# Optimization experiments

Measured on AMD Instinct MI355X. Metric: run time of the kernel, lower is better.

The kernel has to match this reference:

```python
import jax, jax.numpy as jnp
import numpy as np

B, CF, CC, H, W = 4, 64, 128, 512, 512
NUM_POINTS = 4096
OVERSAMPLE = 3
BETA = 0.75
HIDDEN = 256
OUT_CH = 4
IN_FEATS = CF + CC


def grid_sample_points(img, coords):
    """Bilinear sample img [B,C,H,W] at coords [B,N,2] in [0,1] (x,y order),
    matching F.grid_sample(align_corners=False, padding_mode='zeros') after
    the 2*coords-1 normalization in point_sample."""
    Bb, C, Hh, Ww = img.shape
    # unnormalize: ((2c-1)+1)*size/2 - 0.5 == c*size - 0.5
    x = coords[..., 0] * Ww - 0.5
    y = coords[..., 1] * Hh - 0.5
    x0 = jnp.floor(x)
    y0 = jnp.floor(y)
    wx1 = x - x0  # [B,N]
    wy1 = y - y0
    x0i = x0.astype(jnp.int32)
    y0i = y0.astype(jnp.int32)
    flat = img.reshape(Bb, C, Hh * Ww)

    def gather(xi, yi):
        valid = (xi >= 0) & (xi < Ww) & (yi >= 0) & (yi < Hh)
        idx = jnp.clip(yi, 0, Hh - 1) * Ww + jnp.clip(xi, 0, Ww - 1)
        v = jnp.take_along_axis(flat, idx[:, None, :], axis=2)  # [B,C,N]
        return v * valid[:, None, :].astype(img.dtype)

    out = (gather(x0i, y0i) * ((1.0 - wx1) * (1.0 - wy1))[:, None, :]
           + gather(x0i + 1, y0i) * (wx1 * (1.0 - wy1))[:, None, :]
           + gather(x0i, y0i + 1) * ((1.0 - wx1) * wy1)[:, None, :]
           + gather(x0i + 1, y0i + 1) * (wx1 * wy1)[:, None, :])
    return out  # [B,C,N]


def setup_inputs() -> dict:
    key = jax.random.key(0)
    ks = jax.random.split(key, 12)
    num_sampled = NUM_POINTS * OVERSAMPLE
    num_uncertain = int(BETA * NUM_POINTS)
    num_random = NUM_POINTS - num_uncertain
    s1 = 1.0 / np.sqrt(IN_FEATS)
    s2 = 1.0 / np.sqrt(HIDDEN)
    return {
        "fine_features": jax.random.normal(ks[0], (B, CF, H, W), jnp.float32),
        "coarse_features": jax.random.normal(ks[1], (B, CC, H, W), jnp.float32),
        "coarse_logits": jax.random.normal(ks[2], (B, OUT_CH, H, W), jnp.float32),
        "rand_points": jax.random.uniform(ks[3], (B, num_sampled, 2), jnp.float32),
        "rand_extra": jax.random.uniform(ks[4], (B, num_random, 2), jnp.float32),
        "W1": jax.random.uniform(ks[5], (HIDDEN, IN_FEATS), jnp.float32, -s1, s1),
        "b1": jax.random.uniform(ks[6], (HIDDEN,), jnp.float32, -s1, s1),
        "W2": jax.random.uniform(ks[7], (HIDDEN, HIDDEN), jnp.float32, -s2, s2),
        "b2": jax.random.uniform(ks[8], (HIDDEN,), jnp.float32, -s2, s2),
        "W3": jax.random.uniform(ks[9], (OUT_CH, HIDDEN), jnp.float32, -s2, s2),
        "b3": jax.random.uniform(ks[10], (OUT_CH,), jnp.float32, -s2, s2),
    }


def reference(fine_features, coarse_features, coarse_logits, rand_points,
              rand_extra, W1, b1, W2, b2, W3, b3):
    # 1) uncertainty at oversampled random points (channel 0 of coarse logits)
    pt_logits0 = grid_sample_points(coarse_logits, rand_points)[:, 0, :]  # [B,Ns]
    uncertainty = 1.0 - jnp.abs(jax.nn.sigmoid(pt_logits0) - 0.5) * 2.0
    num_uncertain = int(BETA * NUM_POINTS)
    _, idx = jax.lax.top_k(uncertainty, num_uncertain)  # [B,k]
    chosen_uncertain = jnp.take_along_axis(rand_points, idx[..., None], axis=1)
    points = jnp.concatenate([chosen_uncertain, rand_extra], axis=1)  # [B,N,2]
    # 2) gather fine + coarse features at selected points
    fine_s = grid_sample_points(fine_features, points)      # [B,Cf,N]
    coarse_s = grid_sample_points(coarse_features, points)  # [B,Cc,N]
    feats = jnp.concatenate([fine_s, coarse_s], axis=1).transpose(0, 2, 1)  # [B,N,Cin]
    # 3) pointwise MLP (torch Linear: x @ W.T + b)
    h = jax.nn.relu(feats @ W1.T + b1)
    h = jax.nn.relu(h @ W2.T + b2)
    point_logits = (h @ W3.T + b3).transpose(0, 2, 1)  # [B,out_ch,N]
    return point_logits, points
```

## Files before the change

kernel.cpp:

```cpp
#include <hip/hip_runtime.h>
#include <math.h>

#define BATCH 4
#define HW 512
#define NPLANE (512 * 512)
#define NS 12288
#define NU 3072
#define NR 1024
#define NP 4096
#define CF_CH 64
#define CC_CH 128
#define CIN 192
#define HID 256
#define OUTC 4
#define M_TOT (BATCH * NP)
#define GCH_SPLIT 4

__device__ __forceinline__ float xla_expf(float xin) {
  float x = fminf(fmaxf(xin, -88.3762626647949f), 88.3762626647950f);
  float fx = floorf(__fadd_rn(__fmul_rn(x, 1.44269504088896341f), 0.5f));
  float tmp = __fmul_rn(0.693359375f, fx);
  float z = __fmul_rn(-2.12194440e-4f, fx);
  x = __fsub_rn(__fsub_rn(x, tmp), z);
  float y = __fadd_rn(__fmul_rn(x, 1.9875691500E-4f), 1.3981999507E-3f);
  y = __fadd_rn(__fmul_rn(y, x), 8.3334519073E-3f);
  y = __fadd_rn(__fmul_rn(y, x), 4.1665795894E-2f);
  y = __fadd_rn(__fmul_rn(y, x), 1.6666665459E-1f);
  y = __fadd_rn(__fmul_rn(y, x), 5.0000001201E-1f);
  z = __fmul_rn(x, x);
  y = __fadd_rn(__fmul_rn(y, z), x);
  y = __fadd_rn(y, 1.0f);
  int n = (int)fx;
  float p2n = __int_as_float((n + 127) << 23);
  return __fmul_rn(y, p2n);
}

__global__ void k_uncert(const float* __restrict__ logits,
                         const float* __restrict__ rp,
                         float* __restrict__ u) {
  int gid = blockIdx.x * 256 + threadIdx.x;
  if (gid >= BATCH * NS) return;
  int b = gid / NS;
  float px = rp[(size_t)gid * 2 + 0];
  float py = rp[(size_t)gid * 2 + 1];
  const float* plane = logits + (size_t)b * OUTC * NPLANE;

  float x = __fsub_rn(__fmul_rn(px, 512.0f), 0.5f);
  float y = __fsub_rn(__fmul_rn(py, 512.0f), 0.5f);
  float x0f = floorf(x), y0f = floorf(y);
  float wx = __fsub_rn(x, x0f);
  float wy = __fsub_rn(y, y0f);
  int x0 = (int)x0f, y0 = (int)y0f;
  int x1 = x0 + 1, y1 = y0 + 1;
  bool vx0 = (x0 >= 0) & (x0 < HW);
  bool vx1 = (x1 >= 0) & (x1 < HW);
  bool vy0 = (y0 >= 0) & (y0 < HW);
  bool vy1 = (y1 >= 0) & (y1 < HW);
  float g00 = (vx0 && vy0) ? plane[y0 * HW + x0] : 0.0f;
  float g10 = (vx1 && vy0) ? plane[y0 * HW + x1] : 0.0f;
  float g01 = (vx0 && vy1) ? plane[y1 * HW + x0] : 0.0f;
  float g11 = (vx1 && vy1) ? plane[y1 * HW + x1] : 0.0f;
  float omx = __fsub_rn(1.0f, wx);
  float omy = __fsub_rn(1.0f, wy);
  float w00 = __fmul_rn(omx, omy);
  float w10 = __fmul_rn(wx, omy);
  float w01 = __fmul_rn(omx, wy);
  float w11 = __fmul_rn(wx, wy);
  float s = __fadd_rn(
      __fadd_rn(__fadd_rn(__fmul_rn(g00, w00), __fmul_rn(g10, w10)),
                __fmul_rn(g01, w01)),
      __fmul_rn(g11, w11));
  float e = xla_expf(-s);
  float sig = __fdiv_rn(1.0f, __fadd_rn(1.0f, e));
  float t = __fmul_rn(fabsf(__fsub_rn(sig, 0.5f)), 2.0f);
  u[gid] = __fsub_rn(1.0f, t);
}

__global__ __launch_bounds__(256) void k_select(const float* __restrict__ u,
                                                const float* __restrict__ rp,
                                                float* __restrict__ pts_out) {
  __shared__ __align__(16) float su[NS];
  int b = blockIdx.x / (NS / 256);
  int blk = blockIdx.x % (NS / 256);
  const float* ub = u + (size_t)b * NS;
  for (int t = threadIdx.x; t < NS / 4; t += 256)
    ((float4*)su)[t] = ((const float4*)ub)[t];
  __syncthreads();
  int i = blk * 256 + (int)threadIdx.x;
  int wb = i & ~63;
  float ui = su[i];
  int r0 = 0, r1 = 0, r2 = 0, r3 = 0;
  for (int j = 0; j < wb; j += 8) {
    float4 v = *(const float4*)&su[j];
    float4 w = *(const float4*)&su[j + 4];
    r0 += (v.x >= ui) + (w.x >= ui);
    r1 += (v.y >= ui) + (w.y >= ui);
    r2 += (v.z >= ui) + (w.z >= ui);
    r3 += (v.w >= ui) + (w.w >= ui);
  }
  for (int j = wb; j < wb + 64; ++j) {
    float vj = su[j];
    r0 += (vj > ui) || (vj == ui && j < i);
  }
  for (int j = wb + 64; j < NS; j += 8) {
    float4 v = *(const float4*)&su[j];
    float4 w = *(const float4*)&su[j + 4];
    r0 += (v.x > ui) + (w.x > ui);
    r1 += (v.y > ui) + (w.y > ui);
    r2 += (v.z > ui) + (w.z > ui);
    r3 += (v.w > ui) + (w.w > ui);
  }
  int rank = (r0 + r1) + (r2 + r3);
  if (rank < NU) {
    pts_out[((size_t)b * NP + rank) * 2 + 0] = rp[((size_t)b * NS + i) * 2 + 0];
    pts_out[((size_t)b * NP + rank) * 2 + 1] = rp[((size_t)b * NS + i) * 2 + 1];
  }
}

__global__ void k_extra(const float* __restrict__ re, float* __restrict__ pts_out) {
  int gid = blockIdx.x * 256 + threadIdx.x;
  if (gid >= BATCH * NR) return;
  int b = gid / NR, j = gid % NR;
  pts_out[((size_t)b * NP + NU + j) * 2 + 0] = re[(size_t)gid * 2 + 0];
  pts_out[((size_t)b * NP + NU + j) * 2 + 1] = re[(size_t)gid * 2 + 1];
}

__global__ void k_prep(const float* __restrict__ pts, int2* __restrict__ m2,
                       float4* __restrict__ wts) {
  int g = blockIdx.x * 256 + threadIdx.x;
  if (g >= M_TOT) return;
  float px = pts[(size_t)g * 2 + 0];
  float py = pts[(size_t)g * 2 + 1];
  float x = px * 512.0f - 0.5f;
  float y = py * 512.0f - 0.5f;
  float x0f = floorf(x), y0f = floorf(y);
  float wx = x - x0f, wy = y - y0f;
  int x0 = (int)x0f, y0 = (int)y0f;
  bool vx0 = (unsigned)x0 < (unsigned)HW;
  bool vx1 = (unsigned)(x0 + 1) < (unsigned)HW;
  bool vy0 = (unsigned)y0 < (unsigned)HW;
  bool vy1 = (unsigned)(y0 + 1) < (unsigned)HW;
  int vm = (int)(vx0 && vy0) | ((int)(vx1 && vy0) << 1) |
           ((int)(vx0 && vy1) << 2) | ((int)(vx1 && vy1) << 3);
  m2[g] = make_int2(y0 * HW + x0, vm);
  wts[g] = make_float4((1.0f - wx) * (1.0f - wy), wx * (1.0f - wy),
                       (1.0f - wx) * wy, wx * wy);
}

__global__ __launch_bounds__(512) void k_sort(const int2* __restrict__ m2,
                                              int* __restrict__ perm) {
  __shared__ int hist[512], pref[512];
  int b = blockIdx.x, tid = threadIdx.x;
  hist[tid] = 0;
  __syncthreads();
  for (int p = tid; p < NP; p += 512) {
    int i00 = m2[(size_t)b * NP + p].x;
    int key = min(max(i00, 0), NPLANE - 1) >> 9;
    atomicAdd(&hist[key], 1);
  }
  __syncthreads();
  int v = hist[tid];
  pref[tid] = v;
  __syncthreads();
  for (int d = 1; d < 512; d <<= 1) {
    int t = (tid >= d) ? pref[tid - d] : 0;
    __syncthreads();
    pref[tid] += t;
    __syncthreads();
  }
  hist[tid] = pref[tid] - v;
  __syncthreads();
  for (int p = tid; p < NP; p += 512) {
    int i00 = m2[(size_t)b * NP + p].x;
    int key = min(max(i00, 0), NPLANE - 1) >> 9;
    int pos = atomicAdd(&hist[key], 1);
    perm[(size_t)b * NP + pos] = p;
  }
}

__global__ void k_reorder(const int* __restrict__ perm,
                          const int2* __restrict__ m2,
                          const float4* __restrict__ wts,
                          int2* __restrict__ m2s, float4* __restrict__ wtss) {
  int gid = blockIdx.x * 256 + threadIdx.x;
  if (gid >= M_TOT) return;
  int b = gid / NP;
  int p = perm[gid];
  m2s[gid] = m2[(size_t)b * NP + p];
  wtss[gid] = wts[(size_t)b * NP + p];
}

__global__ __launch_bounds__(256) void k_gather5(
    const float* __restrict__ fine, const float* __restrict__ coarse,
    const int2* __restrict__ m2s, const float4* __restrict__ wtss,
    float* __restrict__ featsT) {
  int c = blockIdx.x % CIN;
  int rem = blockIdx.x / CIN;
  int b = rem & (BATCH - 1);
  int part = rem >> 2;
  const float* plane = (c < CF_CH)
                           ? fine + ((size_t)b * CF_CH + c) * NPLANE
                           : coarse + ((size_t)b * CC_CH + (c - CF_CH)) * NPLANE;
  const int2* m2b = m2s + (size_t)b * NP;
  const float4* wtsb = wtss + (size_t)b * NP;
  float* outrow = featsT + (size_t)c * M_TOT + (size_t)b * NP;
  int s0 = part * (NP / GCH_SPLIT);
#pragma unroll
  for (int q = 0; q < NP / GCH_SPLIT / 256; ++q) {
    int s = s0 + q * 256 + (int)threadIdx.x;
    int2 mm = m2b[s];
    float4 w = wtsb[s];
    const float* bp = plane + mm.x;
    float t00 = 0.0f, t10 = 0.0f, t01 = 0.0f, t11 = 0.0f;
    if (mm.y & 1) t00 = bp[0] * w.x;
    if (mm.y & 2) t10 = bp[1] * w.y;
    if (mm.y & 4) t01 = bp[HW] * w.z;
    if (mm.y & 8) t11 = bp[HW + 1] * w.w;
    outrow[s] = ((t00 + t10) + t01) + t11;
  }
}

__global__ __launch_bounds__(256) void k_gemm1_At(const float* __restrict__ At,
                                                  const float* __restrict__ W,
                                                  const float* __restrict__ bias,
                                                  float* __restrict__ C) {
  __shared__ __align__(16) float As[32][68];
  __shared__ __align__(16) float Bs[32][68];
  const int bx = blockIdx.x & 3;
  const int by = blockIdx.x >> 2;
  const int tid = threadIdx.x;
  const int tn = tid & 15, tm = tid >> 4;
  const int m_base = by * 64, n_base = bx * 64;
  float acc[4][4] = {};
  for (int k0 = 0; k0 < CIN; k0 += 32) {
#pragma unroll
    for (int r = 0; r < 2; ++r) {
      int t = tid + r * 256;
      int kk = t >> 4, mg = (t & 15) * 4;
      *(float4*)&As[kk][mg] =
          *(const float4*)&At[(size_t)(k0 + kk) * M_TOT + m_base + mg];
      int row = t >> 3, cg = (t & 7) * 4;
      float4 vw = *(const float4*)&W[(size_t)(n_base + row) * CIN + k0 + cg];
      Bs[cg + 0][row] = vw.x;
      Bs[cg + 1][row] = vw.y;
      Bs[cg + 2][row] = vw.z;
      Bs[cg + 3][row] = vw.w;
    }
    __syncthreads();
#pragma unroll
    for (int kk = 0; kk < 32; ++kk) {
      float4 a4 = *(const float4*)&As[kk][tm * 4];
      float4 b4 = *(const float4*)&Bs[kk][tn * 4];
      float av[4] = {a4.x, a4.y, a4.z, a4.w};
      float bw[4] = {b4.x, b4.y, b4.z, b4.w};
#pragma unroll
      for (int i = 0; i < 4; ++i)
#pragma unroll
        for (int j = 0; j < 4; ++j) acc[i][j] = fmaf(av[i], bw[j], acc[i][j]);
    }
    __syncthreads();
  }
  float bs[4];
#pragma unroll
  for (int j = 0; j < 4; ++j) bs[j] = bias[n_base + tn * 4 + j];
#pragma unroll
  for (int i = 0; i < 4; ++i) {
    float4 o;
    o.x = fmaxf(acc[i][0] + bs[0], 0.0f);
    o.y = fmaxf(acc[i][1] + bs[1], 0.0f);
    o.z = fmaxf(acc[i][2] + bs[2], 0.0f);
    o.w = fmaxf(acc[i][3] + bs[3], 0.0f);
    *(float4*)&C[(size_t)(m_base + tm * 4 + i) * HID + n_base + tn * 4] = o;
  }
}

template <int K>
__global__ __launch_bounds__(256) void k_gemm_relu(const float* __restrict__ A,
                                                   const float* __restrict__ W,
                                                   const float* __restrict__ bias,
                                                   float* __restrict__ C) {
  __shared__ __align__(16) float As[32][68];
  __shared__ __align__(16) float Bs[32][68];
  const int bx = blockIdx.x & 3;
  const int by = blockIdx.x >> 2;
  const int tid = threadIdx.x;
  const int tn = tid & 15, tm = tid >> 4;
  const int m_base = by * 64, n_base = bx * 64;
  float acc[4][4] = {};
  for (int k0 = 0; k0 < K; k0 += 32) {
#pragma unroll
    for (int r = 0; r < 2; ++r) {
      int t = tid + r * 256;
      int row = t >> 3, cg = (t & 7) * 4;
      float4 va = *(const float4*)&A[(size_t)(m_base + row) * K + k0 + cg];
      As[cg + 0][row] = va.x;
      As[cg + 1][row] = va.y;
      As[cg + 2][row] = va.z;
      As[cg + 3][row] = va.w;
      float4 vw = *(const float4*)&W[(size_t)(n_base + row) * K + k0 + cg];
      Bs[cg + 0][row] = vw.x;
      Bs[cg + 1][row] = vw.y;
      Bs[cg + 2][row] = vw.z;
      Bs[cg + 3][row] = vw.w;
    }
    __syncthreads();
#pragma unroll
    for (int kk = 0; kk < 32; ++kk) {
      float4 a4 = *(const float4*)&As[kk][tm * 4];
      float4 b4 = *(const float4*)&Bs[kk][tn * 4];
      float av[4] = {a4.x, a4.y, a4.z, a4.w};
      float bw[4] = {b4.x, b4.y, b4.z, b4.w};
#pragma unroll
      for (int i = 0; i < 4; ++i)
#pragma unroll
        for (int j = 0; j < 4; ++j) acc[i][j] = fmaf(av[i], bw[j], acc[i][j]);
    }
    __syncthreads();
  }
  float bs[4];
#pragma unroll
  for (int j = 0; j < 4; ++j) bs[j] = bias[n_base + tn * 4 + j];
#pragma unroll
  for (int i = 0; i < 4; ++i) {
    float4 o;
    o.x = fmaxf(acc[i][0] + bs[0], 0.0f);
    o.y = fmaxf(acc[i][1] + bs[1], 0.0f);
    o.z = fmaxf(acc[i][2] + bs[2], 0.0f);
    o.w = fmaxf(acc[i][3] + bs[3], 0.0f);
    *(float4*)&C[(size_t)(m_base + tm * 4 + i) * HID + n_base + tn * 4] = o;
  }
}

__global__ __launch_bounds__(256) void k_out(const float* __restrict__ h,
                                             const float* __restrict__ W3,
                                             const float* __restrict__ b3,
                                             const int* __restrict__ perm,
                                             float* __restrict__ out) {
  int gp = blockIdx.x * 4 + (threadIdx.x >> 6);
  int lane = threadIdx.x & 63;
  const float* hr = h + (size_t)gp * HID;
  float4 hv = *(const float4*)&hr[lane * 4];
  float s[4];
#pragma unroll
  for (int o = 0; o < 4; ++o) {
    float4 w = *(const float4*)&W3[o * HID + lane * 4];
    s[o] = hv.x * w.x + hv.y * w.y + hv.z * w.z + hv.w * w.w;
  }
#pragma unroll
  for (int off = 32; off; off >>= 1)
#pragma unroll
    for (int o = 0; o < 4; ++o) s[o] += __shfl_xor(s[o], off, 64);
  if (lane == 0) {
    int b = gp / NP, ns = gp % NP;
    int n = perm[(size_t)b * NP + ns];
#pragma unroll
    for (int o = 0; o < 4; ++o)
      out[((size_t)b * OUTC + o) * NP + n] = s[o] + b3[o];
  }
}

extern "C" void kernel_launch(void* const* d_in, const int* in_sizes, int n_in,
                              void* d_out, int out_size, void* d_ws, size_t ws_size,
                              hipStream_t stream) {
  const float* fine = (const float*)d_in[0];
  const float* coarse = (const float*)d_in[1];
  const float* logits = (const float*)d_in[2];
  const float* rand_points = (const float*)d_in[3];
  const float* rand_extra = (const float*)d_in[4];
  const float* W1 = (const float*)d_in[5];
  const float* b1 = (const float*)d_in[6];
  const float* W2 = (const float*)d_in[7];
  const float* b2 = (const float*)d_in[8];
  const float* W3 = (const float*)d_in[9];
  const float* b3 = (const float*)d_in[10];
  float* out = (float*)d_out;

  float* out_logits = out;
  float* out_points = out + (size_t)BATCH * OUTC * NP;

  char* ws = (char*)d_ws;
  float* u = (float*)(ws + 0);
  int2* m2 = (int2*)(ws + 196608);
  float4* wts = (float4*)(ws + 327680);
  int2* m2s = (int2*)(ws + 589824);
  float4* wtss = (float4*)(ws + 720896);
  int* perm = (int*)(ws + 983040);
  float* featsT = (float*)(ws + 1048576);
  float* h1 = (float*)(ws + 13631488);
  float* h2 = (float*)(ws + 30408704);

  k_uncert<<<(BATCH * NS + 255) / 256, 256, 0, stream>>>(logits, rand_points, u);
  k_select<<<BATCH * (NS / 256), 256, 0, stream>>>(u, rand_points, out_points);
  k_extra<<<(BATCH * NR + 255) / 256, 256, 0, stream>>>(rand_extra, out_points);
  k_prep<<<(M_TOT + 255) / 256, 256, 0, stream>>>(out_points, m2, wts);
  k_sort<<<BATCH, 512, 0, stream>>>(m2, perm);
  k_reorder<<<(M_TOT + 255) / 256, 256, 0, stream>>>(perm, m2, wts, m2s, wtss);
  k_gather5<<<CIN * BATCH * GCH_SPLIT, 256, 0, stream>>>(fine, coarse, m2s,
                                                         wtss, featsT);
  k_gemm1_At<<<(M_TOT / 64) * 4, 256, 0, stream>>>(featsT, W1, b1, h1);
  k_gemm_relu<HID><<<(M_TOT / 64) * 4, 256, 0, stream>>>(h1, W2, b2, h2);
  k_out<<<M_TOT / 4, 256, 0, stream>>>(h2, W3, b3, perm, out_logits);
}
```

Baseline: 306.0 us.

## Run MLP GEMMs on bf16 MFMA with hi/lo split-precision operands

Replaces the two FP32 SIMT shared-memory GEMMs with MFMA bf16 kernels. Each operand is split into high and low bf16 parts and three MFMAs per tile approximate FP32 accuracy. New conversion kernels transpose and split the gathered features and weights, and the first GEMM writes its output already split for the second. This adds extra launches, extra conversion traffic, and direct global loads with no LDS staging, in exchange for matrix-core throughput.

```diff
diff --git a/kernel.cpp b/kernel.cpp
--- a/kernel.cpp
+++ b/kernel.cpp
@@ -15,6 +15,18 @@
 #define OUTC 4
 #define M_TOT (BATCH * NP)
 #define GCH_SPLIT 4
+
+typedef __attribute__((ext_vector_type(8))) short bf16x8;
+typedef __attribute__((ext_vector_type(4))) float f32x4;
+
+__device__ __forceinline__ unsigned short f32_to_bf16_rne(float f) {
+  unsigned u = __float_as_uint(f);
+  unsigned r = u + 0x7FFFu + ((u >> 16) & 1u);
+  return (unsigned short)(r >> 16);
+}
+__device__ __forceinline__ float bf16_to_f32(unsigned short h) {
+  return __uint_as_float((unsigned)h << 16);
+}
 
 __device__ __forceinline__ float xla_expf(float xin) {
   float x = fminf(fmaxf(xin, -88.3762626647949f), 88.3762626647950f);
@@ -220,114 +232,99 @@
   }
 }
 
-__global__ __launch_bounds__(256) void k_gemm1_At(const float* __restrict__ At,
-                                                  const float* __restrict__ W,
-                                                  const float* __restrict__ bias,
-                                                  float* __restrict__ C) {
-  __shared__ __align__(16) float As[32][68];
-  __shared__ __align__(16) float Bs[32][68];
-  const int bx = blockIdx.x & 3;
-  const int by = blockIdx.x >> 2;
-  const int tid = threadIdx.x;
-  const int tn = tid & 15, tm = tid >> 4;
-  const int m_base = by * 64, n_base = bx * 64;
-  float acc[4][4] = {};
-  for (int k0 = 0; k0 < CIN; k0 += 32) {
-#pragma unroll
-    for (int r = 0; r < 2; ++r) {
-      int t = tid + r * 256;
-      int kk = t >> 4, mg = (t & 15) * 4;
-      *(float4*)&As[kk][mg] =
-          *(const float4*)&At[(size_t)(k0 + kk) * M_TOT + m_base + mg];
-      int row = t >> 3, cg = (t & 7) * 4;
-      float4 vw = *(const float4*)&W[(size_t)(n_base + row) * CIN + k0 + cg];
-      Bs[cg + 0][row] = vw.x;
-      Bs[cg + 1][row] = vw.y;
-      Bs[cg + 2][row] = vw.z;
-      Bs[cg + 3][row] = vw.w;
+__global__ __launch_bounds__(256) void k_convA(const float* __restrict__ featsT,
+                                               unsigned short* __restrict__ AH,
+                                               unsigned short* __restrict__ AL) {
+  __shared__ float t[32][65];
+  int c0 = (blockIdx.x % (CIN / 32)) * 32;
+  int m0 = (blockIdx.x / (CIN / 32)) * 64;
+#pragma unroll
+  for (int it = 0; it < 8; ++it) {
+    int idx = it * 256 + (int)threadIdx.x;
+    int cl = idx >> 6, ml = idx & 63;
+    t[cl][ml] = featsT[(size_t)(c0 + cl) * M_TOT + m0 + ml];
+  }
+  __syncthreads();
+#pragma unroll
+  for (int it = 0; it < 8; ++it) {
+    int idx = it * 256 + (int)threadIdx.x;
+    int ml = idx >> 5, cl = idx & 31;
+    float f = t[cl][ml];
+    unsigned short h = f32_to_bf16_rne(f);
+    unsigned short l = f32_to_bf16_rne(f - bf16_to_f32(h));
+    AH[(size_t)(m0 + ml) * CIN + c0 + cl] = h;
+    AL[(size_t)(m0 + ml) * CIN + c0 + cl] = l;
+  }
+}
+
+__global__ void k_convW(const float* __restrict__ W,
+                        unsigned short* __restrict__ WH,
+                        unsigned short* __restrict__ WL, int n) {
+  int g = blockIdx.x * 256 + threadIdx.x;
+  if (g >= n) return;
+  float f = W[g];
+  unsigned short h = f32_to_bf16_rne(f);
+  WH[g] = h;
+  WL[g] = f32_to_bf16_rne(f - bf16_to_f32(h));
+}
+
+template <int K, bool SPLIT>
+__global__ __launch_bounds__(256) void k_mfma(
+    const unsigned short* __restrict__ AH, const unsigned short* __restrict__ AL,
+    const unsigned short* __restrict__ BH, const unsigned short* __restrict__ BL,
+    const float* __restrict__ bias, float* __restrict__ outF,
+    unsigned short* __restrict__ outH, unsigned short* __restrict__ outL) {
+  int lane = (int)threadIdx.x & 63, w = (int)threadIdx.x >> 6;
+  int m0 = blockIdx.y * 64 + (w >> 1) * 32;
+  int n0 = blockIdx.x * 64 + (w & 1) * 32;
+  int rA = lane & 15, kg = (lane >> 4) * 8;
+  f32x4 acc00 = {}, acc01 = {}, acc10 = {}, acc11 = {};
+  for (int kc = 0; kc < K; kc += 32) {
+    int k = kc + kg;
+    bf16x8 ah0 = *(const bf16x8*)&AH[(size_t)(m0 + rA) * K + k];
+    bf16x8 ah1 = *(const bf16x8*)&AH[(size_t)(m0 + 16 + rA) * K + k];
+    bf16x8 al0 = *(const bf16x8*)&AL[(size_t)(m0 + rA) * K + k];
+    bf16x8 al1 = *(const bf16x8*)&AL[(size_t)(m0 + 16 + rA) * K + k];
+    bf16x8 bh0 = *(const bf16x8*)&BH[(size_t)(n0 + rA) * K + k];
+    bf16x8 bh1 = *(const bf16x8*)&BH[(size_t)(n0 + 16 + rA) * K + k];
+    bf16x8 bl0 = *(const bf16x8*)&BL[(size_t)(n0 + rA) * K + k];
+    bf16x8 bl1 = *(const bf16x8*)&BL[(size_t)(n0 + 16 + rA) * K + k];
+    acc00 = __builtin_amdgcn_mfma_f32_16x16x32_bf16(ah0, bh0, acc00, 0, 0, 0);
+    acc00 = __builtin_amdgcn_mfma_f32_16x16x32_bf16(ah0, bl0, acc00, 0, 0, 0);
+    acc00 = __builtin_amdgcn_mfma_f32_16x16x32_bf16(al0, bh0, acc00, 0, 0, 0);
+    acc01 = __builtin_amdgcn_mfma_f32_16x16x32_bf16(ah0, bh1, acc01, 0, 0, 0);
+    acc01 = __builtin_amdgcn_mfma_f32_16x16x32_bf16(ah0, bl1, acc01, 0, 0, 0);
+    acc01 = __builtin_amdgcn_mfma_f32_16x16x32_bf16(al0, bh1, acc01, 0, 0, 0);
+    acc10 = __builtin_amdgcn_mfma_f32_16x16x32_bf16(ah1, bh0, acc10, 0, 0, 0);
+    acc10 = __builtin_amdgcn_mfma_f32_16x16x32_bf16(ah1, bl0, acc10, 0, 0, 0);
+    acc10 = __builtin_amdgcn_mfma_f32_16x16x32_bf16(al1, bh0, acc10, 0, 0, 0);
+    acc11 = __builtin_amdgcn_mfma_f32_16x16x32_bf16(ah1, bh1, acc11, 0, 0, 0);
+    acc11 = __builtin_amdgcn_mfma_f32_16x16x32_bf16(ah1, bl1, acc11, 0, 0, 0);
+    acc11 = __builtin_amdgcn_mfma_f32_16x16x32_bf16(al1, bh1, acc11, 0, 0, 0);
+  }
+  int cr = (lane >> 4) * 4;
+  int cc = lane & 15;
+  float b0 = bias[n0 + cc], b1v = bias[n0 + 16 + cc];
+#pragma unroll
+  for (int r = 0; r < 4; ++r) {
+#pragma unroll
+    for (int fi = 0; fi < 2; ++fi) {
+      int row = m0 + fi * 16 + cr + r;
+      float v0 = fmaxf((fi ? acc10[r] : acc00[r]) + b0, 0.0f);
+      float v1 = fmaxf((fi ? acc11[r] : acc01[r]) + b1v, 0.0f);
+      if constexpr (SPLIT) {
+        unsigned short h0 = f32_to_bf16_rne(v0);
+        unsigned short h1 = f32_to_bf16_rne(v1);
+        outH[(size_t)row * HID + n0 + cc] = h0;
+        outH[(size_t)row * HID + n0 + 16 + cc] = h1;
+        outL[(size_t)row * HID + n0 + cc] = f32_to_bf16_rne(v0 - bf16_to_f32(h0));
+        outL[(size_t)row * HID + n0 + 16 + cc] =
+            f32_to_bf16_rne(v1 - bf16_to_f32(h1));
+      } else {
+        outF[(size_t)row * HID + n0 + cc] = v0;
+        outF[(size_t)row * HID + n0 + 16 + cc] = v1;
+      }
     }
-    __syncthreads();
-#pragma unroll
-    for (int kk = 0; kk < 32; ++kk) {
-      float4 a4 = *(const float4*)&As[kk][tm * 4];
-      float4 b4 = *(const float4*)&Bs[kk][tn * 4];
-      float av[4] = {a4.x, a4.y, a4.z, a4.w};
-      float bw[4] = {b4.x, b4.y, b4.z, b4.w};
-#pragma unroll
-      for (int i = 0; i < 4; ++i)
-#pragma unroll
-        for (int j = 0; j < 4; ++j) acc[i][j] = fmaf(av[i], bw[j], acc[i][j]);
-    }
-    __syncthreads();
-  }
-  float bs[4];
-#pragma unroll
-  for (int j = 0; j < 4; ++j) bs[j] = bias[n_base + tn * 4 + j];
-#pragma unroll
-  for (int i = 0; i < 4; ++i) {
-    float4 o;
-    o.x = fmaxf(acc[i][0] + bs[0], 0.0f);
-    o.y = fmaxf(acc[i][1] + bs[1], 0.0f);
-    o.z = fmaxf(acc[i][2] + bs[2], 0.0f);
-    o.w = fmaxf(acc[i][3] + bs[3], 0.0f);
-    *(float4*)&C[(size_t)(m_base + tm * 4 + i) * HID + n_base + tn * 4] = o;
-  }
-}
-
-template <int K>
-__global__ __launch_bounds__(256) void k_gemm_relu(const float* __restrict__ A,
-                                                   const float* __restrict__ W,
-                                                   const float* __restrict__ bias,
-                                                   float* __restrict__ C) {
-  __shared__ __align__(16) float As[32][68];
-  __shared__ __align__(16) float Bs[32][68];
-  const int bx = blockIdx.x & 3;
-  const int by = blockIdx.x >> 2;
-  const int tid = threadIdx.x;
-  const int tn = tid & 15, tm = tid >> 4;
-  const int m_base = by * 64, n_base = bx * 64;
-  float acc[4][4] = {};
-  for (int k0 = 0; k0 < K; k0 += 32) {
-#pragma unroll
-    for (int r = 0; r < 2; ++r) {
-      int t = tid + r * 256;
-      int row = t >> 3, cg = (t & 7) * 4;
-      float4 va = *(const float4*)&A[(size_t)(m_base + row) * K + k0 + cg];
-      As[cg + 0][row] = va.x;
-      As[cg + 1][row] = va.y;
-      As[cg + 2][row] = va.z;
-      As[cg + 3][row] = va.w;
-      float4 vw = *(const float4*)&W[(size_t)(n_base + row) * K + k0 + cg];
-      Bs[cg + 0][row] = vw.x;
-      Bs[cg + 1][row] = vw.y;
-      Bs[cg + 2][row] = vw.z;
-      Bs[cg + 3][row] = vw.w;
-    }
-    __syncthreads();
-#pragma unroll
-    for (int kk = 0; kk < 32; ++kk) {
-      float4 a4 = *(const float4*)&As[kk][tm * 4];
-      float4 b4 = *(const float4*)&Bs[kk][tn * 4];
-      float av[4] = {a4.x, a4.y, a4.z, a4.w};
-      float bw[4] = {b4.x, b4.y, b4.z, b4.w};
-#pragma unroll
-      for (int i = 0; i < 4; ++i)
-#pragma unroll
-        for (int j = 0; j < 4; ++j) acc[i][j] = fmaf(av[i], bw[j], acc[i][j]);
-    }
-    __syncthreads();
-  }
-  float bs[4];
-#pragma unroll
-  for (int j = 0; j < 4; ++j) bs[j] = bias[n_base + tn * 4 + j];
-#pragma unroll
-  for (int i = 0; i < 4; ++i) {
-    float4 o;
-    o.x = fmaxf(acc[i][0] + bs[0], 0.0f);
-    o.y = fmaxf(acc[i][1] + bs[1], 0.0f);
-    o.z = fmaxf(acc[i][2] + bs[2], 0.0f);
-    o.w = fmaxf(acc[i][3] + bs[3], 0.0f);
-    *(float4*)&C[(size_t)(m_base + tm * 4 + i) * HID + n_base + tn * 4] = o;
   }
 }
 
@@ -386,10 +383,19 @@
   float4* wtss = (float4*)(ws + 720896);
   int* perm = (int*)(ws + 983040);
   float* featsT = (float*)(ws + 1048576);
-  float* h1 = (float*)(ws + 13631488);
-  float* h2 = (float*)(ws + 30408704);
+  unsigned short* AH = (unsigned short*)(ws + 13631488);
+  unsigned short* AL = (unsigned short*)(ws + 19922944);
+  unsigned short* W1H = (unsigned short*)(ws + 26214400);
+  unsigned short* W1L = (unsigned short*)(ws + 26312704);
+  unsigned short* W2H = (unsigned short*)(ws + 26411008);
+  unsigned short* W2L = (unsigned short*)(ws + 26542080);
+  unsigned short* h1H = (unsigned short*)(ws + 26673152);
+  unsigned short* h1L = (unsigned short*)(ws + 35061760);
+  float* h2 = (float*)(ws + 43450368);
 
   k_uncert<<<(BATCH * NS + 255) / 256, 256, 0, stream>>>(logits, rand_points, u);
+  k_convW<<<(HID * CIN + 255) / 256, 256, 0, stream>>>(W1, W1H, W1L, HID * CIN);
+  k_convW<<<(HID * HID + 255) / 256, 256, 0, stream>>>(W2, W2H, W2L, HID * HID);
   k_select<<<BATCH * (NS / 256), 256, 0, stream>>>(u, rand_points, out_points);
   k_extra<<<(BATCH * NR + 255) / 256, 256, 0, stream>>>(rand_extra, out_points);
   k_prep<<<(M_TOT + 255) / 256, 256, 0, stream>>>(out_points, m2, wts);
@@ -397,7 +403,10 @@
   k_reorder<<<(M_TOT + 255) / 256, 256, 0, stream>>>(perm, m2, wts, m2s, wtss);
   k_gather5<<<CIN * BATCH * GCH_SPLIT, 256, 0, stream>>>(fine, coarse, m2s,
                                                          wtss, featsT);
-  k_gemm1_At<<<(M_TOT / 64) * 4, 256, 0, stream>>>(featsT, W1, b1, h1);
-  k_gemm_relu<HID><<<(M_TOT / 64) * 4, 256, 0, stream>>>(h1, W2, b2, h2);
+  k_convA<<<(CIN / 32) * (M_TOT / 64), 256, 0, stream>>>(featsT, AH, AL);
+  k_mfma<CIN, true><<<dim3(HID / 64, M_TOT / 64), 256, 0, stream>>>(
+      AH, AL, W1H, W1L, b1, nullptr, h1H, h1L);
+  k_mfma<HID, false><<<dim3(HID / 64, M_TOT / 64), 256, 0, stream>>>(
+      h1H, h1L, W2H, W2L, b2, h2, nullptr, nullptr);
   k_out<<<M_TOT / 4, 256, 0, stream>>>(h2, W3, b3, perm, out_logits);
 }
```

New measurement: 315.5 us. +3.1%, slower.

## Fuse second MLP GEMM with output projection and merge extra-points copy into uncertainty kernel

Applied to the files above, without the earlier changes.

The second hidden-layer GEMM now computes a full 64x256 tile per block and applies bias, ReLU and the 4-channel output projection in registers. Partial sums are reduced with shuffles, so the h2 buffer round trip and the separate k_out launch go away. The rand_extra copy is folded into the uncertainty kernel, removing one more launch. In exchange the GEMM grid shrinks from 1024 to 256 blocks, each with 64 accumulators per thread and a larger shared tile, which may reduce occupancy and parallelism.

```diff
diff --git a/kernel.cpp b/kernel.cpp
--- a/kernel.cpp
+++ b/kernel.cpp
@@ -35,45 +35,55 @@
   return __fmul_rn(y, p2n);
 }
 
-__global__ void k_uncert(const float* __restrict__ logits,
-                         const float* __restrict__ rp,
-                         float* __restrict__ u) {
+__global__ void k_uncert_extra(const float* __restrict__ logits,
+                               const float* __restrict__ rp,
+                               const float* __restrict__ re,
+                               float* __restrict__ u,
+                               float* __restrict__ pts_out) {
   int gid = blockIdx.x * 256 + threadIdx.x;
-  if (gid >= BATCH * NS) return;
-  int b = gid / NS;
-  float px = rp[(size_t)gid * 2 + 0];
-  float py = rp[(size_t)gid * 2 + 1];
-  const float* plane = logits + (size_t)b * OUTC * NPLANE;
-
-  float x = __fsub_rn(__fmul_rn(px, 512.0f), 0.5f);
-  float y = __fsub_rn(__fmul_rn(py, 512.0f), 0.5f);
-  float x0f = floorf(x), y0f = floorf(y);
-  float wx = __fsub_rn(x, x0f);
-  float wy = __fsub_rn(y, y0f);
-  int x0 = (int)x0f, y0 = (int)y0f;
-  int x1 = x0 + 1, y1 = y0 + 1;
-  bool vx0 = (x0 >= 0) & (x0 < HW);
-  bool vx1 = (x1 >= 0) & (x1 < HW);
-  bool vy0 = (y0 >= 0) & (y0 < HW);
-  bool vy1 = (y1 >= 0) & (y1 < HW);
-  float g00 = (vx0 && vy0) ? plane[y0 * HW + x0] : 0.0f;
-  float g10 = (vx1 && vy0) ? plane[y0 * HW + x1] : 0.0f;
-  float g01 = (vx0 && vy1) ? plane[y1 * HW + x0] : 0.0f;
-  float g11 = (vx1 && vy1) ? plane[y1 * HW + x1] : 0.0f;
-  float omx = __fsub_rn(1.0f, wx);
-  float omy = __fsub_rn(1.0f, wy);
-  float w00 = __fmul_rn(omx, omy);
-  float w10 = __fmul_rn(wx, omy);
-  float w01 = __fmul_rn(omx, wy);
-  float w11 = __fmul_rn(wx, wy);
-  float s = __fadd_rn(
-      __fadd_rn(__fadd_rn(__fmul_rn(g00, w00), __fmul_rn(g10, w10)),
-                __fmul_rn(g01, w01)),
-      __fmul_rn(g11, w11));
-  float e = xla_expf(-s);
-  float sig = __fdiv_rn(1.0f, __fadd_rn(1.0f, e));
-  float t = __fmul_rn(fabsf(__fsub_rn(sig, 0.5f)), 2.0f);
-  u[gid] = __fsub_rn(1.0f, t);
+  if (gid < BATCH * NS) {
+    int b = gid / NS;
+    float px = rp[(size_t)gid * 2 + 0];
+    float py = rp[(size_t)gid * 2 + 1];
+    const float* plane = logits + (size_t)b * OUTC * NPLANE;
+
+    float x = __fsub_rn(__fmul_rn(px, 512.0f), 0.5f);
+    float y = __fsub_rn(__fmul_rn(py, 512.0f), 0.5f);
+    float x0f = floorf(x), y0f = floorf(y);
+    float wx = __fsub_rn(x, x0f);
+    float wy = __fsub_rn(y, y0f);
+    int x0 = (int)x0f, y0 = (int)y0f;
+    int x1 = x0 + 1, y1 = y0 + 1;
+    bool vx0 = (x0 >= 0) & (x0 < HW);
+    bool vx1 = (x1 >= 0) & (x1 < HW);
+    bool vy0 = (y0 >= 0) & (y0 < HW);
+    bool vy1 = (y1 >= 0) & (y1 < HW);
+    float g00 = (vx0 && vy0) ? plane[y0 * HW + x0] : 0.0f;
+    float g10 = (vx1 && vy0) ? plane[y0 * HW + x1] : 0.0f;
+    float g01 = (vx0 && vy1) ? plane[y1 * HW + x0] : 0.0f;
+    float g11 = (vx1 && vy1) ? plane[y1 * HW + x1] : 0.0f;
+    float omx = __fsub_rn(1.0f, wx);
+    float omy = __fsub_rn(1.0f, wy);
+    float w00 = __fmul_rn(omx, omy);
+    float w10 = __fmul_rn(wx, omy);
+    float w01 = __fmul_rn(omx, wy);
+    float w11 = __fmul_rn(wx, wy);
+    float s = __fadd_rn(
+        __fadd_rn(__fadd_rn(__fmul_rn(g00, w00), __fmul_rn(g10, w10)),
+                  __fmul_rn(g01, w01)),
+        __fmul_rn(g11, w11));
+    float e = xla_expf(-s);
+    float sig = __fdiv_rn(1.0f, __fadd_rn(1.0f, e));
+    float t = __fmul_rn(fabsf(__fsub_rn(sig, 0.5f)), 2.0f);
+    u[gid] = __fsub_rn(1.0f, t);
+  } else {
+    int g = gid - BATCH * NS;
+    if (g < BATCH * NR) {
+      int b = g / NR, j = g - b * NR;
+      pts_out[((size_t)b * NP + NU + j) * 2 + 0] = re[(size_t)g * 2 + 0];
+      pts_out[((size_t)b * NP + NU + j) * 2 + 1] = re[(size_t)g * 2 + 1];
+    }
+  }
 }
 
 __global__ __launch_bounds__(256) void k_select(const float* __restrict__ u,
@@ -117,14 +127,6 @@
   }
 }
 
-__global__ void k_extra(const float* __restrict__ re, float* __restrict__ pts_out) {
-  int gid = blockIdx.x * 256 + threadIdx.x;
-  if (gid >= BATCH * NR) return;
-  int b = gid / NR, j = gid % NR;
-  pts_out[((size_t)b * NP + NU + j) * 2 + 0] = re[(size_t)gid * 2 + 0];
-  pts_out[((size_t)b * NP + NU + j) * 2 + 1] = re[(size_t)gid * 2 + 1];
-}
-
 __global__ void k_prep(const float* __restrict__ pts, int2* __restrict__ m2,
                        float4* __restrict__ wts) {
   int g = blockIdx.x * 256 + threadIdx.x;
@@ -274,30 +276,36 @@
   }
 }
 
-template <int K>
-__global__ __launch_bounds__(256) void k_gemm_relu(const float* __restrict__ A,
-                                                   const float* __restrict__ W,
-                                                   const float* __restrict__ bias,
-                                                   float* __restrict__ C) {
+__global__ __launch_bounds__(256) void k_gemm2_fused(
+    const float* __restrict__ A,
+    const float* __restrict__ W,
+    const float* __restrict__ bias,
+    const float* __restrict__ W3,
+    const float* __restrict__ b3,
+    const int* __restrict__ perm,
+    float* __restrict__ out) {
   __shared__ __align__(16) float As[32][68];
-  __shared__ __align__(16) float Bs[32][68];
-  const int bx = blockIdx.x & 3;
-  const int by = blockIdx.x >> 2;
+  __shared__ __align__(16) float Bs[32][260];
   const int tid = threadIdx.x;
-  const int tn = tid & 15, tm = tid >> 4;
-  const int m_base = by * 64, n_base = bx * 64;
-  float acc[4][4] = {};
-  for (int k0 = 0; k0 < K; k0 += 32) {
+  const int tm = tid >> 4, tn = tid & 15;
+  const int m_base = blockIdx.x * 64;
+  float acc[4][16] = {};
+  for (int k0 = 0; k0 < HID; k0 += 32) {
 #pragma unroll
     for (int r = 0; r < 2; ++r) {
       int t = tid + r * 256;
       int row = t >> 3, cg = (t & 7) * 4;
-      float4 va = *(const float4*)&A[(size_t)(m_base + row) * K + k0 + cg];
+      float4 va = *(const float4*)&A[(size_t)(m_base + row) * HID + k0 + cg];
       As[cg + 0][row] = va.x;
       As[cg + 1][row] = va.y;
       As[cg + 2][row] = va.z;
       As[cg + 3][row] = va.w;
-      float4 vw = *(const float4*)&W[(size_t)(n_base + row) * K + k0 + cg];
+    }
+#pragma unroll
+    for (int r = 0; r < 8; ++r) {
+      int t = tid + r * 256;
+      int row = t >> 3, cg = (t & 7) * 4;
+      float4 vw = *(const float4*)&W[(size_t)row * HID + k0 + cg];
       Bs[cg + 0][row] = vw.x;
       Bs[cg + 1][row] = vw.y;
       Bs[cg + 2][row] = vw.z;
@@ -306,56 +314,51 @@
     __syncthreads();
 #pragma unroll
     for (int kk = 0; kk < 32; ++kk) {
-      float4 a4 = *(const float4*)&As[kk][tm * 4];
-      float4 b4 = *(const float4*)&Bs[kk][tn * 4];
-      float av[4] = {a4.x, a4.y, a4.z, a4.w};
-      float bw[4] = {b4.x, b4.y, b4.z, b4.w};
+      float a4[4];
+      *(float4*)a4 = *(const float4*)&As[kk][tm * 4];
+      float bw[16];
+#pragma unroll
+      for (int j = 0; j < 4; ++j)
+        *(float4*)&bw[j * 4] = *(const float4*)&Bs[kk][tn * 16 + j * 4];
 #pragma unroll
       for (int i = 0; i < 4; ++i)
 #pragma unroll
-        for (int j = 0; j < 4; ++j) acc[i][j] = fmaf(av[i], bw[j], acc[i][j]);
-    }
-    __syncthreads();
-  }
-  float bs[4];
-#pragma unroll
-  for (int j = 0; j < 4; ++j) bs[j] = bias[n_base + tn * 4 + j];
-#pragma unroll
-  for (int i = 0; i < 4; ++i) {
-    float4 o;
-    o.x = fmaxf(acc[i][0] + bs[0], 0.0f);
-    o.y = fmaxf(acc[i][1] + bs[1], 0.0f);
-    o.z = fmaxf(acc[i][2] + bs[2], 0.0f);
-    o.w = fmaxf(acc[i][3] + bs[3], 0.0f);
-    *(float4*)&C[(size_t)(m_base + tm * 4 + i) * HID + n_base + tn * 4] = o;
-  }
-}
-
-__global__ __launch_bounds__(256) void k_out(const float* __restrict__ h,
-                                             const float* __restrict__ W3,
-                                             const float* __restrict__ b3,
-                                             const int* __restrict__ perm,
-                                             float* __restrict__ out) {
-  int gp = blockIdx.x * 4 + (threadIdx.x >> 6);
-  int lane = threadIdx.x & 63;
-  const float* hr = h + (size_t)gp * HID;
-  float4 hv = *(const float4*)&hr[lane * 4];
-  float s[4];
-#pragma unroll
-  for (int o = 0; o < 4; ++o) {
-    float4 w = *(const float4*)&W3[o * HID + lane * 4];
-    s[o] = hv.x * w.x + hv.y * w.y + hv.z * w.z + hv.w * w.w;
-  }
-#pragma unroll
-  for (int off = 32; off; off >>= 1)
-#pragma unroll
-    for (int o = 0; o < 4; ++o) s[o] += __shfl_xor(s[o], off, 64);
-  if (lane == 0) {
-    int b = gp / NP, ns = gp % NP;
-    int n = perm[(size_t)b * NP + ns];
-#pragma unroll
-    for (int o = 0; o < 4; ++o)
-      out[((size_t)b * OUTC + o) * NP + n] = s[o] + b3[o];
+        for (int j = 0; j < 16; ++j)
+          acc[i][j] = fmaf(a4[i], bw[j], acc[i][j]);
+    }
+    __syncthreads();
+  }
+  float p[4][4] = {};
+#pragma unroll
+  for (int j = 0; j < 16; ++j) {
+    int n = tn * 16 + j;
+    float bn = bias[n];
+    float w3v[4];
+#pragma unroll
+    for (int o = 0; o < 4; ++o) w3v[o] = W3[o * HID + n];
+#pragma unroll
+    for (int i = 0; i < 4; ++i) {
+      float h = fmaxf(acc[i][j] + bn, 0.0f);
+#pragma unroll
+      for (int o = 0; o < 4; ++o) p[i][o] = fmaf(h, w3v[o], p[i][o]);
+    }
+  }
+#pragma unroll
+  for (int off = 8; off; off >>= 1)
+#pragma unroll
+    for (int i = 0; i < 4; ++i)
+#pragma unroll
+      for (int o = 0; o < 4; ++o) p[i][o] += __shfl_xor(p[i][o], off, 64);
+  if (tn == 0) {
+    int b = (int)blockIdx.x / (NP / 64);
+#pragma unroll
+    for (int i = 0; i < 4; ++i) {
+      int ms = m_base + tm * 4 + i;
+      int n = perm[(size_t)b * NP + (ms - b * NP)];
+#pragma unroll
+      for (int o = 0; o < 4; ++o)
+        out[((size_t)b * OUTC + o) * NP + n] = p[i][o] + b3[o];
+    }
   }
 }
 
@@ -387,17 +390,16 @@
   int* perm = (int*)(ws + 983040);
   float* featsT = (float*)(ws + 1048576);
   float* h1 = (float*)(ws + 13631488);
-  float* h2 = (float*)(ws + 30408704);
-
-  k_uncert<<<(BATCH * NS + 255) / 256, 256, 0, stream>>>(logits, rand_points, u);
+
+  k_uncert_extra<<<(BATCH * NS + BATCH * NR + 255) / 256, 256, 0, stream>>>(
+      logits, rand_points, rand_extra, u, out_points);
   k_select<<<BATCH * (NS / 256), 256, 0, stream>>>(u, rand_points, out_points);
-  k_extra<<<(BATCH * NR + 255) / 256, 256, 0, stream>>>(rand_extra, out_points);
   k_prep<<<(M_TOT + 255) / 256, 256, 0, stream>>>(out_points, m2, wts);
   k_sort<<<BATCH, 512, 0, stream>>>(m2, perm);
   k_reorder<<<(M_TOT + 255) / 256, 256, 0, stream>>>(perm, m2, wts, m2s, wtss);
   k_gather5<<<CIN * BATCH * GCH_SPLIT, 256, 0, stream>>>(fine, coarse, m2s,
                                                          wtss, featsT);
   k_gemm1_At<<<(M_TOT / 64) * 4, 256, 0, stream>>>(featsT, W1, b1, h1);
-  k_gemm_relu<HID><<<(M_TOT / 64) * 4, 256, 0, stream>>>(h1, W2, b2, h2);
-  k_out<<<M_TOT / 4, 256, 0, stream>>>(h2, W3, b3, perm, out_logits);
-}
+  k_gemm2_fused<<<M_TOT / 64, 256, 0, stream>>>(h1, W2, b2, W3, b3, perm,
+                                                out_logits);
+}
```

Measured after the change: 310.5 us. No clear change (+1.5%).
